# Performance work log

Measured on AMD Instinct MI355X. Metric: run time of the kernel, lower is better.

The kernel has to match this reference:

```python
import jax, jax.numpy as jnp
import numpy as np

SIGMA = 0.005  # hard-coded in naive_corres


def _neg_sqdist(x, y):
    # -||x_i - y_j||^2 via GEMM expansion; x:[B,N,D], y:[B,M,D] -> [B,N,M]
    x2 = jnp.sum(x * x, axis=-1)  # [B,N]
    y2 = jnp.sum(y * y, axis=-1)  # [B,M]
    xy = jnp.einsum('bnd,bmd->bnm', x, y)
    return -(x2[:, :, None] + y2[:, None, :] - 2.0 * xy)


def setup_inputs() -> dict:
    key = jax.random.key(0)
    k1, k2, k3, k4 = jax.random.split(key, 4)
    B, N, D = 2, 4096, 32
    points = jax.random.uniform(k1, (B, N, 3), dtype=jnp.float32)
    pointfea1 = jax.random.normal(k2, (B, N, D), dtype=jnp.float32)
    pointfea2 = jax.random.normal(k3, (B, N, D), dtype=jnp.float32)
    weights = jax.random.uniform(k4, (B, N, 1), dtype=jnp.float32) / N
    return {"points": points, "pointfea1": pointfea1,
            "pointfea2": pointfea2, "weights": weights}


def reference(points, pointfea1, pointfea2, weights):
    # --- naive_corres ---
    p = points / SIGMA
    point_dist2 = _neg_sqdist(p, p)                       # [B,N,N]
    point_loggauss = jax.nn.log_softmax(point_dist2, axis=2)
    fea_dist2 = _neg_sqdist(pointfea1, pointfea2)         # [B,N,N]
    fea_logsoftmax = jax.nn.log_softmax(fea_dist2, axis=2)
    # ce per source point, weighted, summed over points -> [B]
    ce = -jnp.sum(jnp.exp(point_loggauss) * fea_logsoftmax, axis=2)  # [B,N]
    ce_loss = jnp.sum(ce * weights[..., 0], axis=1)       # [B]
    # --- reg_loss (pos_is_in_fea=True -> skip first 3 channels) ---
    reg = (pointfea1[:, :, 3:] ** 2 + pointfea2[:, :, 3:] ** 2)
    reg_loss = reg.mean(axis=2).mean(axis=1)              # [B]
    return ce_loss, reg_loss
```

## Files before the change

### kernel.cpp

```cpp
#include <hip/hip_runtime.h>
#include <math.h>


#define NPTS 4096
#define ROWS_TOT 8192
#define DF 32

#define L2E  1.4426950408889634f
#define LN2  0.6931471805599453f
#define FSC  1.6986436f
#define PSC  240.2244f

typedef _Float16 half8 __attribute__((ext_vector_type(8)));
typedef float f4 __attribute__((ext_vector_type(4)));

__global__ void kA_prep(const float* __restrict__ pts,
                        const float* __restrict__ f1g,
                        const float* __restrict__ f2g,
                        float* __restrict__ pp1, float* __restrict__ pp2,
                        _Float16* __restrict__ fragA, _Float16* __restrict__ fragB,
                        float* __restrict__ regp, float* __restrict__ out) {
    const int r = blockIdx.x * 64 + threadIdx.x;
    if (r < 4) out[r] = 0.0f;
    const int jt = r >> 4;
    const int c  = r & 15;

    float n1, n2, reg1, reg2;
    {
        const float4* f2v = (const float4*)(f2g + (size_t)r * DF);
        float vals[32];
        float s = 0.0f;
#pragma unroll
        for (int q = 0; q < 8; ++q) {
            float4 v = f2v[q];
            vals[4*q]=v.x; vals[4*q+1]=v.y; vals[4*q+2]=v.z; vals[4*q+3]=v.w;
            s += v.x*v.x + v.y*v.y + v.z*v.z + v.w*v.w;
        }
        n2 = s;
        reg2 = s - vals[0]*vals[0] - vals[1]*vals[1] - vals[2]*vals[2];
        half8* fv = (half8*)fragB;
#pragma unroll
        for (int kb = 0; kb < 4; ++kb) {
            half8 h;
#pragma unroll
            for (int i = 0; i < 8; ++i) h[i] = (_Float16)(vals[kb*8+i] * FSC);
            fv[(size_t)jt*64 + kb*16 + c] = h;
        }
    }
    {
        const float4* f1v = (const float4*)(f1g + (size_t)r * DF);
        float vals[32];
        float s = 0.0f;
#pragma unroll
        for (int q = 0; q < 8; ++q) {
            float4 v = f1v[q];
            vals[4*q]=v.x; vals[4*q+1]=v.y; vals[4*q+2]=v.z; vals[4*q+3]=v.w;
            s += v.x*v.x + v.y*v.y + v.z*v.z + v.w*v.w;
        }
        n1 = s;
        reg1 = s - vals[0]*vals[0] - vals[1]*vals[1] - vals[2]*vals[2];
        half8* fv = (half8*)fragA;
#pragma unroll
        for (int kb = 0; kb < 4; ++kb) {
            half8 h;
#pragma unroll
            for (int i = 0; i < 8; ++i) h[i] = (_Float16)(vals[kb*8+i] * FSC);
            fv[(size_t)jt*64 + kb*16 + c] = h;
        }
    }
    const float* pp = pts + (size_t)r * 3;
    const float px = pp[0]*PSC, py = pp[1]*PSC, pz = pp[2]*PSC;
    ((float4*)pp1)[r] = make_float4(px, py, pz, n1 * L2E);
    ((float4*)pp2)[r] = make_float4(px, py, pz, n2 * L2E);
    regp[r] = reg1 + reg2;
}

__launch_bounds__(512)
__global__ void kB_main(const float* __restrict__ pp1,
                        const float* __restrict__ pp2,
                        const _Float16* __restrict__ fragA,
                        const _Float16* __restrict__ fragB,
                        float* __restrict__ part) {
    __shared__ float sS[8][32], sT[8][32], sF[8][32];

    const int tid = threadIdx.x;
    const int l = tid & 63, wv = tid >> 6;
    const int ip = blockIdx.x >> 1;
    const int jh = blockIdx.x & 1;
    const int b  = ip >> 7;
    const int i0g = ip * 32;
    const int lr = l & 15, lk = l >> 4;

    const half8 afA = ((const half8*)fragA)[(size_t)(ip * 2)     * 64 + l];
    const half8 afB = ((const half8*)fragA)[(size_t)(ip * 2 + 1) * 64 + l];

    const int rbA = i0g + lk * 4;
    const int rbB = i0g + 16 + lk * 4;
    f4 qxA, qyA, qzA, qwA, qxB, qyB, qzB, qwB;
#pragma unroll
    for (int e = 0; e < 4; ++e) {
        const float4 qA = ((const float4*)pp1)[rbA + e];
        const float4 qB = ((const float4*)pp1)[rbB + e];
        qxA[e] = qA.x; qyA[e] = qA.y; qzA[e] = qA.z; qwA[e] = qA.w;
        qxB[e] = qB.x; qyB[e] = qB.y; qzB[e] = qB.z; qwB[e] = qB.w;
    }

    const int jt0 = b * 256 + jh * 128 + wv * 16;
    const int j0  = b * NPTS + jh * 2048 + wv * 256 + lr;
    const half8*  fbase = (const half8*)fragB + ((size_t)jt0 * 64 + l);
    const float4* pbase = (const float4*)pp2 + j0;

    f4 spA = {0,0,0,0}, tAA = {0,0,0,0}, sfA = {0,0,0,0};
    f4 spB = {0,0,0,0}, tAB = {0,0,0,0}, sfB = {0,0,0,0};
    const f4 zero = {0.f, 0.f, 0.f, 0.f};

    half8  bfC = fbase[0];
    float4 pwC = pbase[0];
#pragma unroll
    for (int t = 0; t < 16; ++t) {
        half8  bfN = bfC;
        float4 pwN = pwC;
        if (t < 15) {
            bfN = fbase[(t + 1) * 64];
            pwN = pbase[(t + 1) * 16];
        }
        const f4 ccA = __builtin_amdgcn_mfma_f32_16x16x32_f16(afA, bfC, zero, 0, 0, 0);
        const f4 ccB = __builtin_amdgcn_mfma_f32_16x16x32_f16(afB, bfC, zero, 0, 0, 0);
        {
            const f4 fd = ccA - qwA - pwC.w;
            const f4 dx = qxA - pwC.x;
            const f4 dy = qyA - pwC.y;
            const f4 dz = qzA - pwC.z;
            const f4 s  = dx*dx + dy*dy + dz*dz;
            f4 ep, ef;
#pragma unroll
            for (int e = 0; e < 4; ++e) {
                ep[e] = __builtin_amdgcn_exp2f(-s[e]);
                ef[e] = __builtin_amdgcn_exp2f(fd[e]);
            }
            spA += ep; tAA += ep * fd; sfA += ef;
        }
        {
            const f4 fd = ccB - qwB - pwC.w;
            const f4 dx = qxB - pwC.x;
            const f4 dy = qyB - pwC.y;
            const f4 dz = qzB - pwC.z;
            const f4 s  = dx*dx + dy*dy + dz*dz;
            f4 ep, ef;
#pragma unroll
            for (int e = 0; e < 4; ++e) {
                ep[e] = __builtin_amdgcn_exp2f(-s[e]);
                ef[e] = __builtin_amdgcn_exp2f(fd[e]);
            }
            spB += ep; tAB += ep * fd; sfB += ef;
        }
        bfC = bfN;
        pwC = pwN;
    }

#pragma unroll
    for (int m = 1; m < 16; m <<= 1) {
#pragma unroll
        for (int e = 0; e < 4; ++e) {
            spA[e] += __shfl_xor(spA[e], m);
            tAA[e] += __shfl_xor(tAA[e], m);
            sfA[e] += __shfl_xor(sfA[e], m);
            spB[e] += __shfl_xor(spB[e], m);
            tAB[e] += __shfl_xor(tAB[e], m);
            sfB[e] += __shfl_xor(sfB[e], m);
        }
    }
    if (lr == 0) {
#pragma unroll
        for (int e = 0; e < 4; ++e) {
            sS[wv][lk * 4 + e]      = spA[e];
            sT[wv][lk * 4 + e]      = tAA[e];
            sF[wv][lk * 4 + e]      = sfA[e];
            sS[wv][16 + lk * 4 + e] = spB[e];
            sT[wv][16 + lk * 4 + e] = tAB[e];
            sF[wv][16 + lk * 4 + e] = sfB[e];
        }
    }
    __syncthreads();

    if (tid < 32) {
        float sp_ = 0.f, tp_ = 0.f, sf_ = 0.f;
#pragma unroll
        for (int w = 0; w < 8; ++w) {
            sp_ += sS[w][tid];
            tp_ += sT[w][tid];
            sf_ += sF[w][tid];
        }
        float* P = part + (size_t)jh * 3 * ROWS_TOT;
        P[i0g + tid]                = sp_;
        P[ROWS_TOT + i0g + tid]     = tp_;
        P[2 * ROWS_TOT + i0g + tid] = sf_;
    }
}

__global__ void k2_final(const float* __restrict__ part,
                         const float* __restrict__ regp,
                         const float* __restrict__ wg,
                         float* __restrict__ out) {
    __shared__ float redc[4], redr[4];
    const int tid = threadIdx.x;
    const int r = blockIdx.x * 256 + tid;
    const int b = r >> 12;

    const float* P0 = part;
    const float* P1 = part + (size_t)3 * ROWS_TOT;
    const float sp_ = P0[r] + P1[r];
    const float tp_ = P0[ROWS_TOT + r] + P1[ROWS_TOT + r];
    const float sf_ = P0[2*ROWS_TOT + r] + P1[2*ROWS_TOT + r];
    const float ce = __logf(sf_) - (tp_ * LN2) / sp_;
    float contrib = wg[r] * ce;
    float rr = regp[r];

#pragma unroll
    for (int off = 32; off > 0; off >>= 1) {
        contrib += __shfl_down(contrib, off);
        rr      += __shfl_down(rr, off);
    }
    const int wave = tid >> 6, lane = tid & 63;
    if (lane == 0) { redc[wave] = contrib; redr[wave] = rr; }
    __syncthreads();
    if (tid == 0) {
        atomicAdd(&out[b],     redc[0] + redc[1] + redc[2] + redc[3]);
        atomicAdd(&out[2 + b], (redr[0] + redr[1] + redr[2] + redr[3])
                               * (1.0f / (29.0f * (float)NPTS)));
    }
}

extern "C" void kernel_launch(void* const* d_in, const int* in_sizes, int n_in,
                              void* d_out, int out_size, void* d_ws, size_t ws_size,
                              hipStream_t stream) {
    const float* pts = (const float*)d_in[0];
    const float* f1  = (const float*)d_in[1];
    const float* f2  = (const float*)d_in[2];
    const float* wg  = (const float*)d_in[3];
    float* out = (float*)d_out;

    float* ws = (float*)d_ws;
    float*     pp1   = ws;
    float*     pp2   = ws + 32768;
    _Float16*  fragB = (_Float16*)(ws + 65536);
    _Float16*  fragA = (_Float16*)(ws + 196608);
    float*     regp  = ws + 327680;
    float*     part  = ws + 335872;

    kA_prep<<<ROWS_TOT / 64, 64, 0, stream>>>(pts, f1, f2, pp1, pp2,
                                              fragA, fragB, regp, out);
    kB_main<<<512, 512, 0, stream>>>(pp1, pp2, fragA, fragB, part);
    k2_final<<<ROWS_TOT / 256, 256, 0, stream>>>(part, regp, wg, out);
}
```

Baseline: 28.53 us.

## Compute point distances on MFMA via split-fp16 GEMM with norms folded into accumulator

The spatial squared distance is now computed as a matrix product on the MFMA units. Coordinates are split into fp16 high and low parts so that the cross terms h*h, h*l and l*h keep precision, and the norm terms are fed through the MFMA accumulator input. Feature norms are likewise folded into the MFMA C operand, which removes the per-element VALU subtract and squared-distance math in the inner loop. The cost is twice as many MFMA calls, larger fragment buffers with a 128-stride layout, and some precision risk because the point coordinates are scaled to about 340, so the high/low fp16 split and the cancellation in the exponent may lose accuracy.

```diff
diff --git a/kernel.cpp b/kernel.cpp
--- a/kernel.cpp
+++ b/kernel.cpp
@@ -9,7 +9,7 @@
 #define L2E  1.4426950408889634f
 #define LN2  0.6931471805599453f
 #define FSC  1.6986436f
-#define PSC  240.2244f
+#define PSC2 339.72872f
 
 typedef _Float16 half8 __attribute__((ext_vector_type(8)));
 typedef float f4 __attribute__((ext_vector_type(4)));
@@ -17,7 +17,7 @@
 __global__ void kA_prep(const float* __restrict__ pts,
                         const float* __restrict__ f1g,
                         const float* __restrict__ f2g,
-                        float* __restrict__ pp1, float* __restrict__ pp2,
+                        float2* __restrict__ nrm1, float2* __restrict__ nrm2,
                         _Float16* __restrict__ fragA, _Float16* __restrict__ fragB,
                         float* __restrict__ regp, float* __restrict__ out) {
     const int r = blockIdx.x * 64 + threadIdx.x;
@@ -28,8 +28,7 @@
     float n1, n2, reg1, reg2;
     {
         const float4* f2v = (const float4*)(f2g + (size_t)r * DF);
-        float vals[32];
-        float s = 0.0f;
+        float vals[32]; float s = 0.0f;
 #pragma unroll
         for (int q = 0; q < 8; ++q) {
             float4 v = f2v[q];
@@ -44,13 +43,12 @@
             half8 h;
 #pragma unroll
             for (int i = 0; i < 8; ++i) h[i] = (_Float16)(vals[kb*8+i] * FSC);
-            fv[(size_t)jt*64 + kb*16 + c] = h;
+            fv[(size_t)jt*128 + kb*16 + c] = h;
         }
     }
     {
         const float4* f1v = (const float4*)(f1g + (size_t)r * DF);
-        float vals[32];
-        float s = 0.0f;
+        float vals[32]; float s = 0.0f;
 #pragma unroll
         for (int q = 0; q < 8; ++q) {
             float4 v = f1v[q];
@@ -65,19 +63,45 @@
             half8 h;
 #pragma unroll
             for (int i = 0; i < 8; ++i) h[i] = (_Float16)(vals[kb*8+i] * FSC);
-            fv[(size_t)jt*64 + kb*16 + c] = h;
-        }
-    }
-    const float* pp = pts + (size_t)r * 3;
-    const float px = pp[0]*PSC, py = pp[1]*PSC, pz = pp[2]*PSC;
-    ((float4*)pp1)[r] = make_float4(px, py, pz, n1 * L2E);
-    ((float4*)pp2)[r] = make_float4(px, py, pz, n2 * L2E);
+            fv[(size_t)jt*128 + kb*16 + c] = h;
+        }
+    }
+    {
+        const float* pp = pts + (size_t)r * 3;
+        const float v0 = pp[0]*PSC2, v1 = pp[1]*PSC2, v2 = pp[2]*PSC2;
+        const float h0 = (float)(_Float16)v0, h1 = (float)(_Float16)v1,
+                    h2 = (float)(_Float16)v2;
+        const float l0 = v0 - h0, l1 = v1 - h1, l2 = v2 - h2;
+        const float np = 0.5f * (v0*v0 + v1*v1 + v2*v2);
+
+        const float pa[16] = {h0,h1,h2,h0,h1,h2,l0,l1,  l2,l0,l1,l2,0,0,0,0};
+        const float pb[16] = {h0,h1,h2,l0,l1,l2,h0,h1,  h2,l0,l1,l2,0,0,0,0};
+        half8* fa = (half8*)fragA;
+        half8* fb = (half8*)fragB;
+#pragma unroll
+        for (int kb = 0; kb < 2; ++kb) {
+            half8 ha, hb;
+#pragma unroll
+            for (int i = 0; i < 8; ++i) {
+                ha[i] = (_Float16)pa[kb*8+i];
+                hb[i] = (_Float16)pb[kb*8+i];
+            }
+            fa[(size_t)jt*128 + 64 + kb*16 + c] = ha;
+            fb[(size_t)jt*128 + 64 + kb*16 + c] = hb;
+        }
+        const half8 z = {0,0,0,0,0,0,0,0};
+        fa[(size_t)jt*128 + 64 + 32 + c] = z;  fa[(size_t)jt*128 + 64 + 48 + c] = z;
+        fb[(size_t)jt*128 + 64 + 32 + c] = z;  fb[(size_t)jt*128 + 64 + 48 + c] = z;
+
+        nrm1[r] = make_float2(-(n1 * L2E), -np);
+        nrm2[r] = make_float2(  n2 * L2E,   np);
+    }
     regp[r] = reg1 + reg2;
 }
 
 __launch_bounds__(512)
-__global__ void kB_main(const float* __restrict__ pp1,
-                        const float* __restrict__ pp2,
+__global__ void kB_main(const float2* __restrict__ nrm1,
+                        const float2* __restrict__ nrm2,
                         const _Float16* __restrict__ fragA,
                         const _Float16* __restrict__ fragB,
                         float* __restrict__ part) {
@@ -91,71 +115,69 @@
     const int i0g = ip * 32;
     const int lr = l & 15, lk = l >> 4;
 
-    const half8 afA = ((const half8*)fragA)[(size_t)(ip * 2)     * 64 + l];
-    const half8 afB = ((const half8*)fragA)[(size_t)(ip * 2 + 1) * 64 + l];
+    const half8 afFA = ((const half8*)fragA)[(size_t)(ip*2)   * 128 + l];
+    const half8 afPA = ((const half8*)fragA)[(size_t)(ip*2)   * 128 + 64 + l];
+    const half8 afFB = ((const half8*)fragA)[(size_t)(ip*2+1) * 128 + l];
+    const half8 afPB = ((const half8*)fragA)[(size_t)(ip*2+1) * 128 + 64 + l];
 
     const int rbA = i0g + lk * 4;
     const int rbB = i0g + 16 + lk * 4;
-    f4 qxA, qyA, qzA, qwA, qxB, qyB, qzB, qwB;
+    f4 qfA, qpA, qfB, qpB;
 #pragma unroll
     for (int e = 0; e < 4; ++e) {
-        const float4 qA = ((const float4*)pp1)[rbA + e];
-        const float4 qB = ((const float4*)pp1)[rbB + e];
-        qxA[e] = qA.x; qyA[e] = qA.y; qzA[e] = qA.z; qwA[e] = qA.w;
-        qxB[e] = qB.x; qyB[e] = qB.y; qzB[e] = qB.z; qwB[e] = qB.w;
+        const float2 a = nrm1[rbA + e];
+        const float2 bq = nrm1[rbB + e];
+        qfA[e] = a.x;  qpA[e] = a.y;
+        qfB[e] = bq.x; qpB[e] = bq.y;
     }
 
     const int jt0 = b * 256 + jh * 128 + wv * 16;
     const int j0  = b * NPTS + jh * 2048 + wv * 256 + lr;
-    const half8*  fbase = (const half8*)fragB + ((size_t)jt0 * 64 + l);
-    const float4* pbase = (const float4*)pp2 + j0;
+    const half8*  fbase = (const half8*)fragB + ((size_t)jt0 * 128 + l);
+    const float2* nbase = nrm2 + j0;
 
     f4 spA = {0,0,0,0}, tAA = {0,0,0,0}, sfA = {0,0,0,0};
     f4 spB = {0,0,0,0}, tAB = {0,0,0,0}, sfB = {0,0,0,0};
-    const f4 zero = {0.f, 0.f, 0.f, 0.f};
-
-    half8  bfC = fbase[0];
-    float4 pwC = pbase[0];
+
+    half8  bfFC = fbase[0];
+    half8  bfPC = fbase[64];
+    float2 nwC  = nbase[0];
 #pragma unroll
     for (int t = 0; t < 16; ++t) {
-        half8  bfN = bfC;
-        float4 pwN = pwC;
+        half8 bfFN = bfFC, bfPN = bfPC;
+        float2 nwN = nwC;
         if (t < 15) {
-            bfN = fbase[(t + 1) * 64];
-            pwN = pbase[(t + 1) * 16];
-        }
-        const f4 ccA = __builtin_amdgcn_mfma_f32_16x16x32_f16(afA, bfC, zero, 0, 0, 0);
-        const f4 ccB = __builtin_amdgcn_mfma_f32_16x16x32_f16(afB, bfC, zero, 0, 0, 0);
+            bfFN = fbase[(t + 1) * 128];
+            bfPN = fbase[(t + 1) * 128 + 64];
+            nwN  = nbase[(t + 1) * 16];
+        }
         {
-            const f4 fd = ccA - qwA - pwC.w;
-            const f4 dx = qxA - pwC.x;
-            const f4 dy = qyA - pwC.y;
-            const f4 dz = qzA - pwC.z;
-            const f4 s  = dx*dx + dy*dy + dz*dz;
+            const f4 C1 = qfA - nwC.x;
+            const f4 C2 = qpA - nwC.y;
+            const f4 fd = __builtin_amdgcn_mfma_f32_16x16x32_f16(afFA, bfFC, C1, 0, 0, 0);
+            const f4 pd = __builtin_amdgcn_mfma_f32_16x16x32_f16(afPA, bfPC, C2, 0, 0, 0);
             f4 ep, ef;
 #pragma unroll
             for (int e = 0; e < 4; ++e) {
-                ep[e] = __builtin_amdgcn_exp2f(-s[e]);
+                ep[e] = __builtin_amdgcn_exp2f(pd[e]);
                 ef[e] = __builtin_amdgcn_exp2f(fd[e]);
             }
             spA += ep; tAA += ep * fd; sfA += ef;
         }
         {
-            const f4 fd = ccB - qwB - pwC.w;
-            const f4 dx = qxB - pwC.x;
-            const f4 dy = qyB - pwC.y;
-            const f4 dz = qzB - pwC.z;
-            const f4 s  = dx*dx + dy*dy + dz*dz;
+            const f4 C1 = qfB - nwC.x;
+            const f4 C2 = qpB - nwC.y;
+            const f4 fd = __builtin_amdgcn_mfma_f32_16x16x32_f16(afFB, bfFC, C1, 0, 0, 0);
+            const f4 pd = __builtin_amdgcn_mfma_f32_16x16x32_f16(afPB, bfPC, C2, 0, 0, 0);
             f4 ep, ef;
 #pragma unroll
             for (int e = 0; e < 4; ++e) {
-                ep[e] = __builtin_amdgcn_exp2f(-s[e]);
+                ep[e] = __builtin_amdgcn_exp2f(pd[e]);
                 ef[e] = __builtin_amdgcn_exp2f(fd[e]);
             }
             spB += ep; tAB += ep * fd; sfB += ef;
         }
-        bfC = bfN;
-        pwC = pwN;
+        bfFC = bfFN; bfPC = bfPN; nwC = nwN;
     }
 
 #pragma unroll
@@ -241,15 +263,15 @@
     float* out = (float*)d_out;
 
     float* ws = (float*)d_ws;
-    float*     pp1   = ws;
-    float*     pp2   = ws + 32768;
-    _Float16*  fragB = (_Float16*)(ws + 65536);
-    _Float16*  fragA = (_Float16*)(ws + 196608);
-    float*     regp  = ws + 327680;
-    float*     part  = ws + 335872;
-
-    kA_prep<<<ROWS_TOT / 64, 64, 0, stream>>>(pts, f1, f2, pp1, pp2,
+    float2*    nrm1  = (float2*)ws;
+    float2*    nrm2  = (float2*)(ws + 16384);
+    _Float16*  fragB = (_Float16*)(ws + 32768);
+    _Float16*  fragA = (_Float16*)(ws + 294912);
+    float*     regp  = ws + 557056;
+    float*     part  = ws + 565248;
+
+    kA_prep<<<ROWS_TOT / 64, 64, 0, stream>>>(pts, f1, f2, nrm1, nrm2,
                                               fragA, fragB, regp, out);
-    kB_main<<<512, 512, 0, stream>>>(pp1, pp2, fragA, fragB, part);
+    kB_main<<<512, 512, 0, stream>>>(nrm1, nrm2, fragA, fragB, part);
     k2_final<<<ROWS_TOT / 256, 256, 0, stream>>>(part, regp, wg, out);
 }
```

Measured after the change: 24.91 us, median of 2. 12.7% less time.
